# Kernel tuning notes

Hardware: AMD Instinct MI355X
Metric: run time of the kernel (lower is better)

## Reference

```python
import jax, jax.numpy as jnp
import numpy as np
import math

C_IN, C_OUT = 256, 256
KH, KW = 3, 3
STRIDE, PAD = 1, 1
CURV = 1.0
SQRT_C = math.sqrt(CURV)
EPS = 1e-15

def _beta(a, b):
    return math.exp(math.lgamma(a) + math.lgamma(b) - math.lgamma(a + b))

BETA_NI = _beta(C_IN / 2.0, 0.5)                 # beta(n_i/2, 1/2)
BETA_N = _beta(C_IN * KH * KW / 2.0, 0.5)        # beta(n/2, 1/2)


def logmap0(y, axis):
    n = jnp.maximum(jnp.linalg.norm(y, axis=axis, keepdims=True), EPS)
    return jnp.arctanh(jnp.minimum(SQRT_C * n, 1.0 - 1e-7)) * y / (SQRT_C * n)


def expmap0(v, axis):
    n = jnp.maximum(jnp.linalg.norm(v, axis=axis, keepdims=True), EPS)
    return jnp.tanh(SQRT_C * n) * v / (SQRT_C * n)


def unfold(x):
    # torch.nn.Unfold: x [B,C,H,W] -> [B, C*KH*KW, L], channel-major patch order
    B, C, H, W = x.shape
    Ho = (H + 2 * PAD - KH) // STRIDE + 1
    Wo = (W + 2 * PAD - KW) // STRIDE + 1
    xp = jnp.pad(x, ((0, 0), (0, 0), (PAD, PAD), (PAD, PAD)))
    cols = [xp[:, :, i:i + STRIDE * Ho:STRIDE, j:j + STRIDE * Wo:STRIDE]
            for i in range(KH) for j in range(KW)]
    patches = jnp.stack(cols, axis=2)            # [B, C, KH*KW, Ho, Wo]
    return patches.reshape(B, C * KH * KW, Ho * Wo), Ho, Wo


def poincare_fc(x, z, r):
    # x: [..., D_in] on ball, z: [D_in, D_out], r: [D_out]
    x2 = jnp.sum(x * x, axis=-1, keepdims=True)
    lam = 2.0 / (1.0 - CURV * x2)                # conformal factor lambda_x
    z_norm = jnp.maximum(jnp.linalg.norm(z, axis=0), EPS)  # [D_out]
    xz = x @ z                                   # [..., D_out]
    two_csr = 2.0 * SQRT_C * r
    inner = (SQRT_C * lam * xz / z_norm * jnp.cosh(two_csr)
             - (lam - 1.0) * jnp.sinh(two_csr))
    v = 2.0 * z_norm / SQRT_C * jnp.arcsinh(inner)   # hyperplane distances
    w = jnp.sinh(SQRT_C * v) / SQRT_C
    return w / (1.0 + jnp.sqrt(1.0 + CURV * jnp.sum(w * w, axis=-1, keepdims=True)))


def setup_inputs() -> dict:
    key = jax.random.key(0)
    k1, k2, k3 = jax.random.split(key, 3)
    # tangent vectors -> points on the Poincare ball (man_dim=1)
    v = 0.05 * jax.random.normal(k1, (16, C_IN, 64, 64), dtype=jnp.float32)
    x = expmap0(v, axis=1)
    std = (2.0 * C_IN * KH * KW * C_OUT) ** (-0.5)
    weights = std * jax.random.normal(k2, (KH * KW * C_IN, C_OUT), dtype=jnp.float32)
    bias = 0.01 * jax.random.normal(k3, (C_OUT,), dtype=jnp.float32)
    return {"x": x, "weights": weights, "bias": bias}


def reference(x, weights, bias):
    B = x.shape[0]
    v = logmap0(x, axis=1) * (BETA_N / BETA_NI)      # log map + beta scaling
    u, Ho, Wo = unfold(v)                            # [B, CK, L]
    u = jnp.swapaxes(u, 1, 2)                        # [B, L, CK]
    p = expmap0(u, axis=-1)                          # back onto the ball
    y = poincare_fc(p, weights, bias)                # [B, L, C_OUT]
    return jnp.swapaxes(y, 1, 2).reshape(B, C_OUT, Ho, Wo)
```

## Files before the change

### kernel.cpp

```cpp
#include <hip/hip_runtime.h>
#include <cmath>

typedef __bf16 bf16;
typedef __bf16 bf16x8 __attribute__((ext_vector_type(8)));
typedef float f32x4 __attribute__((ext_vector_type(4)));

#define SBAR() __builtin_amdgcn_sched_barrier(0)


__device__ inline void gload16(const void* g, void* l) {
    __builtin_amdgcn_global_load_lds(
        (const __attribute__((address_space(1))) unsigned int*)g,
        (__attribute__((address_space(3))) unsigned int*)l, 16, 0, 0);
}

__global__ void k_prep_zt(const float* __restrict__ z, bf16* __restrict__ zt5) {
    int s = blockIdx.x;
    int cc = s / 9, tap = s % 9;
    int co = threadIdx.x;
#pragma unroll
    for (int g = 0; g < 4; ++g) {
        bf16x8 pk;
#pragma unroll
        for (int e = 0; e < 8; ++e) {
            int c = cc * 32 + g * 8 + e;
            pk[e] = (bf16)z[(size_t)(c * 9 + tap) * 256 + co];
        }
        *(bf16x8*)(zt5 + ((size_t)(s * 4 + g) * 256 + co) * 8) = pk;
    }
}

__global__ void k_prep_cols(const float* __restrict__ z, const float* __restrict__ r,
                            float* __restrict__ zn, float* __restrict__ ch,
                            float* __restrict__ sh) {
    __shared__ float red[256];
    int co = blockIdx.x, t = threadIdx.x;
    float s = 0.f;
    for (int i = 0; i < 9; ++i) {
        float v = z[(size_t)(i * 256 + t) * 256 + co];
        s += v * v;
    }
    red[t] = s;
    __syncthreads();
    for (int off = 128; off >= 1; off >>= 1) {
        if (t < off) red[t] += red[t + off];
        __syncthreads();
    }
    if (t == 0) {
        zn[co] = fmaxf(sqrtf(red[0]), 1e-15f);
        float tc = 2.f * r[co];
        ch[co] = coshf(tc);
        sh[co] = sinhf(tc);
    }
}

__global__ void k_logmap(const float* __restrict__ x, unsigned int* __restrict__ vt_u,
                         float* __restrict__ sq, float Rbeta) {
    __shared__ float tile[256][33];
    __shared__ float red[8][32];
    __shared__ float afac[32];
    int tid = threadIdx.x;
    int blk = blockIdx.x;
    int b = blk >> 7;
    int pix0 = (blk & 127) << 5;

    for (int it = 0; it < 32; ++it) {
        int c = it * 8 + (tid >> 5);
        int p = tid & 31;
        tile[c][p] = x[((size_t)b * 256 + c) * 4096 + pix0 + p];
    }
    __syncthreads();

    {
        int part = tid >> 5, p = tid & 31;
        float s = 0.f;
        for (int i = 0; i < 32; ++i) {
            float v = tile[part * 32 + i][p];
            s += v * v;
        }
        red[part][p] = s;
    }
    __syncthreads();
    if (tid < 32) {
        float n2 = 0.f;
        for (int i = 0; i < 8; ++i) n2 += red[i][tid];
        float n = sqrtf(n2);
        float nc = fmaxf(n, 1e-15f);
        float a = atanhf(fminf(nc, 0.9999999f)) / nc * Rbeta;
        afac[tid] = a;
        sq[(size_t)b * 4096 + pix0 + tid] = a * a * n2;
    }
    __syncthreads();

    for (int it = 0; it < 16; ++it) {
        int idx = it * 256 + tid;
        int p = idx >> 7;
        int cp = idx & 127;
        float a = afac[p];
        float v0 = a * tile[2 * cp][p];
        float v1 = a * tile[2 * cp + 1][p];
        union { bf16 h[2]; unsigned int u; } pk;
        pk.h[0] = (bf16)v0;
        pk.h[1] = (bf16)v1;
        vt_u[((size_t)b * 4096 + pix0 + p) * 128 + cp] = pk.u;
    }
}

__global__ void
__attribute__((amdgpu_flat_work_group_size(256, 256)))
__attribute__((amdgpu_waves_per_eu(2, 2)))
k_hconv(const bf16* __restrict__ vt, const bf16* __restrict__ zt5,
        const float* __restrict__ sq,
        const float* __restrict__ znp, const float* __restrict__ chp,
        const float* __restrict__ shp, float* __restrict__ out) {
    __shared__ __align__(1024) char Asb[16896];
    __shared__ __align__(1024) char Bb3[3][16448];
    __shared__ float s_lds[128], lam_lds[128];
    __shared__ float red[128][2];

    int tid = threadIdx.x;
    int bid = blockIdx.x;
    int bh = ((bid & 7) << 6) | (bid >> 3);
    int b = bh >> 5, h0 = (bh & 31) << 1;

    if (tid < 32) {
        int u = tid >> 1, side = tid & 1;
        *(f32x4*)(Asb + u * 1056 + side * 1040) = (f32x4){0.f, 0.f, 0.f, 0.f};
    }

    if (tid >= 128) {
        int t = tid - 128;
        int h = h0 + (t >> 6), w = t & 63;
        const float* sb = sq + ((size_t)b << 12);
        float q = 0.f;
#pragma unroll
        for (int dh = -1; dh <= 1; ++dh) {
            int hhh = h + dh;
            if ((unsigned)hhh >= 64u) continue;
#pragma unroll
            for (int dw = -1; dw <= 1; ++dw) {
                int ww = w + dw;
                if ((unsigned)ww >= 64u) continue;
                q += sb[hhh * 64 + ww];
            }
        }
        float ncl = fmaxf(sqrtf(q), 1e-15f);
        float p = __expf(2.f * ncl);
        float tt = (p - 1.f) / (p + 1.f);
        s_lds[t] = tt / ncl;
        lam_lds[t] = 2.f / (1.f - tt * tt);
    }

    int wave = tid >> 6, lane = tid & 63;
    int wn = wave & 1, wm = wave >> 1;
    int lrow = lane & 15, lk = lane >> 4;

    f32x4 acc[4][8];
#pragma unroll
    for (int m = 0; m < 4; ++m)
#pragma unroll
        for (int n = 0; n < 8; ++n) acc[m][n] = (f32x4){0.f, 0.f, 0.f, 0.f};

    const bf16* vb = vt + (((size_t)b) << 12) * 256;

    auto stageA = [&](int ccn) {
#pragma unroll
        for (int it = 0; it < 4; ++it) {
            int u = wave * 4 + it;
            int r = u >> 2, g = u & 3;
            int hr = h0 - 1 + r;
            hr = hr < 0 ? 0 : (hr > 63 ? 63 : hr);
            const bf16* gp = vb + ((size_t)(hr * 64 + lane)) * 256 + ccn * 32 + g * 8;
            gload16(gp, Asb + u * 1056 + 16);
        }
    };
    auto stageB = [&](char* dst, int s) {
        const char* src = (const char*)zt5 + (size_t)s * 16384;
#pragma unroll
        for (int it = 0; it < 4; ++it) {
            gload16(src + it * 4096 + wave * 1024 + lane * 16,
                    dst + it * 4112 + wave * 1024);
        }
    };

    stageB((char*)Bb3[0], 0);
    stageA(0);
    __syncthreads();
    SBAR();

    const char* ApB = Asb + lk * 1056 + lrow * 16;
    const int bOff = lk * 4112 + (wn * 128 + lrow) * 16;

#define STAGE(CCV, TAP)                                                      \
    {                                                                        \
        const int s_ = (CCV) * 9 + (TAP);                                    \
        if (s_ < 71) stageB((char*)Bb3[((TAP) + 1) % 3], s_ + 1);            \
        SBAR();                                                              \
        if (s_ < 71) { asm volatile("s_waitcnt vmcnt(4)" ::: "memory"); }    \
        else         { asm volatile("s_waitcnt vmcnt(0)" ::: "memory"); }    \
        SBAR();                                                              \
        asm volatile("s_barrier" ::: "memory");        \
        SBAR();                                                              \
        {                                                                    \
            const int dh_ = (TAP) / 3 - 1, dw_ = (TAP) % 3 - 1;              \
            int hh_ = h0 + wm + dh_;                                         \
            if ((unsigned)hh_ < 64u) {                                       \
                const char* Ap_ = ApB + (wm + dh_ + 1) * 4224 + (dw_ + 1) * 16; \
                const char* Bp_ = (const char*)Bb3[(TAP) % 3] + bOff;        \
                bf16x8 a0 = *(const bf16x8*)(Ap_);                           \
                bf16x8 a1 = *(const bf16x8*)(Ap_ + 256);                     \
                bf16x8 a2 = *(const bf16x8*)(Ap_ + 512);                     \
                bf16x8 a3 = *(const bf16x8*)(Ap_ + 768);                     \
                __builtin_amdgcn_s_setprio(1);                               \
                _Pragma("unroll")                                            \
                for (int n = 0; n < 8; ++n) {                                \
                    bf16x8 bb = *(const bf16x8*)(Bp_ + n * 256);             \
                    acc[0][n] = __builtin_amdgcn_mfma_f32_16x16x32_bf16(a0, bb, acc[0][n], 0, 0, 0); \
                    acc[1][n] = __builtin_amdgcn_mfma_f32_16x16x32_bf16(a1, bb, acc[1][n], 0, 0, 0); \
                    acc[2][n] = __builtin_amdgcn_mfma_f32_16x16x32_bf16(a2, bb, acc[2][n], 0, 0, 0); \
                    acc[3][n] = __builtin_amdgcn_mfma_f32_16x16x32_bf16(a3, bb, acc[3][n], 0, 0, 0); \
                }                                                            \
                __builtin_amdgcn_s_setprio(0);                               \
            }                                                                \
        }                                                                    \
        if ((TAP) == 8 && (CCV) < 7) {                                       \
            SBAR();                                                          \
            asm volatile("s_barrier" ::: "memory");    \
            SBAR();                                                          \
            stageA((CCV) + 1);                                               \
            SBAR();                                                          \
        }                                                                    \
    }

#pragma unroll 1
    for (int cc = 0; cc < 8; ++cc) {
        STAGE(cc, 0) STAGE(cc, 1) STAGE(cc, 2)
        STAGE(cc, 3) STAGE(cc, 4) STAGE(cc, 5)
        STAGE(cc, 6) STAGE(cc, 7) STAGE(cc, 8)
    }
#undef STAGE

    float cz[8], sh8[8], tz[8];
#pragma unroll
    for (int n = 0; n < 8; ++n) {
        int co = wn * 128 + n * 16 + lrow;
        float zn = znp[co];
        cz[n] = chp[co] / zn;
        sh8[n] = shp[co];
        tz[n] = 2.f * zn;
    }

#pragma unroll
    for (int m = 0; m < 4; ++m) {
#pragma unroll
        for (int r = 0; r < 4; ++r) {
            int wp = wm * 64 + m * 16 + 4 * lk + r;
            float s = s_lds[wp], lam = lam_lds[wp];
            float lm1 = lam - 1.f;
            float psum = 0.f;
#pragma unroll
            for (int n = 0; n < 8; ++n) {
                float xz = s * acc[m][n][r];
                float inner = lam * xz * cz[n] - lm1 * sh8[n];
                float as = __logf(inner + sqrtf(inner * inner + 1.f));
                float p = __expf(tz[n] * as);
                float w = 0.5f * (p - __builtin_amdgcn_rcpf(p));
                acc[m][n][r] = w;
                psum += w * w;
            }
            psum += __shfl_xor(psum, 1);
            psum += __shfl_xor(psum, 2);
            psum += __shfl_xor(psum, 4);
            psum += __shfl_xor(psum, 8);
            if (lrow == 0) red[wp][wn] = psum;
        }
    }
    __syncthreads();

    float dinv[4][4];
#pragma unroll
    for (int m = 0; m < 4; ++m)
#pragma unroll
        for (int r = 0; r < 4; ++r) {
            int wp = wm * 64 + m * 16 + 4 * lk + r;
            float tot = red[wp][0] + red[wp][1];
            dinv[m][r] = __builtin_amdgcn_rcpf(1.f + sqrtf(1.f + tot));
        }

    float* ob = out + (size_t)b * 256 * 4096 + (h0 + wm) * 64;
#pragma unroll
    for (int m = 0; m < 4; ++m) {
#pragma unroll
        for (int n = 0; n < 8; ++n) {
            int co = wn * 128 + n * 16 + lrow;
            f32x4 o;
#pragma unroll
            for (int r = 0; r < 4; ++r) o[r] = acc[m][n][r] * dinv[m][r];
            *(f32x4*)(ob + (size_t)co * 4096 + m * 16 + 4 * lk) = o;
        }
    }
}

extern "C" void kernel_launch(void* const* d_in, const int* in_sizes, int n_in,
                              void* d_out, int out_size, void* d_ws, size_t ws_size,
                              hipStream_t stream) {
    const float* x = (const float*)d_in[0];
    const float* z = (const float*)d_in[1];
    const float* r = (const float*)d_in[2];
    float* out = (float*)d_out;

    char* ws = (char*)d_ws;
    bf16* vt = (bf16*)ws;
    float* sq = (float*)(ws + 33554432);
    bf16* zt5 = (bf16*)(ws + 34078720);
    float* zn = (float*)(ws + 35258368);
    float* ch = (float*)(ws + 35259392);
    float* sh = (float*)(ws + 35260416);
    if (ws_size < 35261440) return;

    double bni = lgamma(128.0) + lgamma(0.5) - lgamma(128.5);
    double bn = lgamma(1152.0) + lgamma(0.5) - lgamma(1152.5);
    float Rbeta = (float)exp(bn - bni);

    k_prep_zt<<<72, 256, 0, stream>>>(z, zt5);
    k_prep_cols<<<256, 256, 0, stream>>>(z, r, zn, ch, sh);
    k_logmap<<<2048, 256, 0, stream>>>(x, (unsigned int*)vt, sq, Rbeta);
    k_hconv<<<512, 256, 0, stream>>>(vt, zt5, sq, zn, ch, sh, out);
}
```

Before: 124.9 us.

## Deepen B-tile prefetch to two stages and double-buffer B fragments in registers

Global-to-LDS prefetch of weight tiles now runs two stages ahead instead of one, using all three LDS buffers. The B fragments for the next tap are read from LDS into registers before the current tap's MFMAs, ping-ponging between two register arrays, so LDS read latency overlaps compute. The channel loop is unrolled by two so the register buffer parity stays static. This adds 64 VGPRs of live fragments, which may lower occupancy or cause spills. The next-buffer read happens after the barrier and could race with the stageB that overwrites that buffer.

```diff
diff --git a/kernel.cpp b/kernel.cpp
--- a/kernel.cpp
+++ b/kernel.cpp
@@ -184,6 +184,7 @@
     };
 
     stageB((char*)Bb3[0], 0);
+    stageB((char*)Bb3[1], 1);
     stageA(0);
     __syncthreads();
     SBAR();
@@ -191,22 +192,37 @@
     const char* ApB = Asb + lk * 1056 + lrow * 16;
     const int bOff = lk * 4112 + (wn * 128 + lrow) * 16;
 
-#define STAGE(CCV, TAP)                                                      \
+    bf16x8 bfA[8], bfB[8];
+#pragma unroll
+    for (int n = 0; n < 8; ++n)
+        bfA[n] = *(const bf16x8*)((const char*)Bb3[0] + bOff + n * 256);
+
+#define STAGE(CCV, TAP, CUR, NXT)                                            \
     {                                                                        \
         const int s_ = (CCV) * 9 + (TAP);                                    \
-        if (s_ < 71) stageB((char*)Bb3[((TAP) + 1) % 3], s_ + 1);            \
+        if (s_ + 2 < 72) stageB((char*)Bb3[((TAP) + 2) % 3], s_ + 2);        \
         SBAR();                                                              \
-        if (s_ < 71) { asm volatile("s_waitcnt vmcnt(4)" ::: "memory"); }    \
+        if (s_ < 70) { asm volatile("s_waitcnt vmcnt(4)" ::: "memory"); }    \
         else         { asm volatile("s_waitcnt vmcnt(0)" ::: "memory"); }    \
         SBAR();                                                              \
-        asm volatile("s_barrier" ::: "memory");        \
+        asm volatile("s_barrier" ::: "memory");     \
         SBAR();                                                              \
+        if (s_ + 1 < 72) {        \
+            const char* Bn_ = (const char*)Bb3[((TAP) + 1) % 3] + bOff;      \
+            NXT[0] = *(const bf16x8*)(Bn_);                                  \
+            NXT[1] = *(const bf16x8*)(Bn_ + 256);                            \
+            NXT[2] = *(const bf16x8*)(Bn_ + 512);                            \
+            NXT[3] = *(const bf16x8*)(Bn_ + 768);                            \
+            NXT[4] = *(const bf16x8*)(Bn_ + 1024);                           \
+            NXT[5] = *(const bf16x8*)(Bn_ + 1280);                           \
+            NXT[6] = *(const bf16x8*)(Bn_ + 1536);                           \
+            NXT[7] = *(const bf16x8*)(Bn_ + 1792);                           \
+        }                                                                    \
         {                                                                    \
             const int dh_ = (TAP) / 3 - 1, dw_ = (TAP) % 3 - 1;              \
             int hh_ = h0 + wm + dh_;                                         \
             if ((unsigned)hh_ < 64u) {                                       \
                 const char* Ap_ = ApB + (wm + dh_ + 1) * 4224 + (dw_ + 1) * 16; \
-                const char* Bp_ = (const char*)Bb3[(TAP) % 3] + bOff;        \
                 bf16x8 a0 = *(const bf16x8*)(Ap_);                           \
                 bf16x8 a1 = *(const bf16x8*)(Ap_ + 256);                     \
                 bf16x8 a2 = *(const bf16x8*)(Ap_ + 512);                     \
@@ -214,11 +230,10 @@
                 __builtin_amdgcn_s_setprio(1);                               \
                 _Pragma("unroll")                                            \
                 for (int n = 0; n < 8; ++n) {                                \
-                    bf16x8 bb = *(const bf16x8*)(Bp_ + n * 256);             \
-                    acc[0][n] = __builtin_amdgcn_mfma_f32_16x16x32_bf16(a0, bb, acc[0][n], 0, 0, 0); \
-                    acc[1][n] = __builtin_amdgcn_mfma_f32_16x16x32_bf16(a1, bb, acc[1][n], 0, 0, 0); \
-                    acc[2][n] = __builtin_amdgcn_mfma_f32_16x16x32_bf16(a2, bb, acc[2][n], 0, 0, 0); \
-                    acc[3][n] = __builtin_amdgcn_mfma_f32_16x16x32_bf16(a3, bb, acc[3][n], 0, 0, 0); \
+                    acc[0][n] = __builtin_amdgcn_mfma_f32_16x16x32_bf16(a0, CUR[n], acc[0][n], 0, 0, 0); \
+                    acc[1][n] = __builtin_amdgcn_mfma_f32_16x16x32_bf16(a1, CUR[n], acc[1][n], 0, 0, 0); \
+                    acc[2][n] = __builtin_amdgcn_mfma_f32_16x16x32_bf16(a2, CUR[n], acc[2][n], 0, 0, 0); \
+                    acc[3][n] = __builtin_amdgcn_mfma_f32_16x16x32_bf16(a3, CUR[n], acc[3][n], 0, 0, 0); \
                 }                                                            \
                 __builtin_amdgcn_s_setprio(0);                               \
             }                                                                \
@@ -233,10 +248,14 @@
     }
 
 #pragma unroll 1
-    for (int cc = 0; cc < 8; ++cc) {
-        STAGE(cc, 0) STAGE(cc, 1) STAGE(cc, 2)
-        STAGE(cc, 3) STAGE(cc, 4) STAGE(cc, 5)
-        STAGE(cc, 6) STAGE(cc, 7) STAGE(cc, 8)
+    for (int cc2 = 0; cc2 < 4; ++cc2) {
+        const int c0 = 2 * cc2, c1 = c0 + 1;
+        STAGE(c0, 0, bfA, bfB) STAGE(c0, 1, bfB, bfA) STAGE(c0, 2, bfA, bfB)
+        STAGE(c0, 3, bfB, bfA) STAGE(c0, 4, bfA, bfB) STAGE(c0, 5, bfB, bfA)
+        STAGE(c0, 6, bfA, bfB) STAGE(c0, 7, bfB, bfA) STAGE(c0, 8, bfA, bfB)
+        STAGE(c1, 0, bfB, bfA) STAGE(c1, 1, bfA, bfB) STAGE(c1, 2, bfB, bfA)
+        STAGE(c1, 3, bfA, bfB) STAGE(c1, 4, bfB, bfA) STAGE(c1, 5, bfA, bfB)
+        STAGE(c1, 6, bfB, bfA) STAGE(c1, 7, bfA, bfB) STAGE(c1, 8, bfB, bfA)
     }
 #undef STAGE
 
```

Measured after the change: 122.4 us. 2.0% less time.
